# Kernel optimization log

Measured on AMD Instinct MI355X. Metric: run time of the kernel, lower is better.

The kernel has to match this reference:

```python
import jax, jax.numpy as jnp
import numpy as np

H, Q, D, V = 256, 64, 512, 34
L, N, T = 1024, 64, 256


def _mlp(x, W0, b0, W1, b1):
    # two-layer MLP with ELU on hidden (matches MLP with nn.ELU activation)
    return jax.nn.elu(x @ W0.T + b0) @ W1.T + b1


def _lstm_cell(x, h, c, Wih, Whh, bih, bhh):
    gates = x @ Wih.T + bih + h @ Whh.T + bhh
    i, f, g, o = jnp.split(gates, 4, axis=-1)  # PyTorch LSTMCell gate order
    i, f, o = jax.nn.sigmoid(i), jax.nn.sigmoid(f), jax.nn.sigmoid(o)
    c_new = f * c + i * jnp.tanh(g)
    h_new = o * jnp.tanh(c_new)
    return h_new, c_new


def _attn(q, key, value, mask):
    # q: [N,Q], key: [N,L,Q], value: [N,L,H], mask: [N,L]
    scores = jnp.einsum('nlq,nq->nl', key, q)
    a = jax.nn.softmax(scores, axis=-1) * mask
    a = a / jnp.sum(a, axis=-1, keepdims=True)
    return jnp.einsum('nl,nlh->nh', a, value)


def setup_inputs() -> dict:
    key = jax.random.key(0)
    ks = iter(jax.random.split(key, 64))

    def rn(shape, s=0.05):
        return jax.random.normal(next(ks), shape, jnp.float32) * s

    inp = {
        'seqs': rn((L, N, D), 1.0),
        'seq_lens': jax.random.randint(next(ks), (N,), L // 2, L + 1),
        'labels': jax.random.randint(next(ks), (T, N), 0, V),
        'emb': rn((V, H)),
        'inith': rn((3, H)),
        'initc': rn((3, H)),
    }
    in_sizes = [2 * H, H, H]
    for i in range(3):
        inp[f'Wih{i}'] = rn((4 * H, in_sizes[i]))
        inp[f'Whh{i}'] = rn((4 * H, H))
        inp[f'bih{i}'] = rn((4 * H,))
        inp[f'bhh{i}'] = rn((4 * H,))
    inp['qW0'] = rn((H, H)); inp['qb0'] = rn((H,))
    inp['qW1'] = rn((Q, H)); inp['qb1'] = rn((Q,))
    inp['kW0'] = rn((D, D)); inp['kb0'] = rn((D,))
    inp['kW1'] = rn((Q, D)); inp['kb1'] = rn((Q,))
    inp['vW0'] = rn((H, D)); inp['vb0'] = rn((H,))
    inp['vW1'] = rn((H, H)); inp['vb1'] = rn((H,))
    inp['outW'] = rn((V, 2 * H)); inp['outb'] = rn((V,))
    return inp


def reference(seqs, seq_lens, labels, emb, inith, initc,
              Wih0, Whh0, bih0, bhh0, Wih1, Whh1, bih1, bhh1,
              Wih2, Whh2, bih2, bhh2,
              qW0, qb0, qW1, qb1, kW0, kb0, kW1, kb1,
              vW0, vb0, vW1, vb1, outW, outb):
    T_, N_ = labels.shape
    L_ = seqs.shape[0]
    lstm = [(Wih0, Whh0, bih0, bhh0), (Wih1, Whh1, bih1, bhh1), (Wih2, Whh2, bih2, bhh2)]

    char_input = emb[labels]                                   # [T,N,H]
    key = _mlp(seqs, kW0, kb0, kW1, kb1).transpose(1, 0, 2)    # [N,L,Q]
    value = _mlp(seqs, vW0, vb0, vW1, vb1).transpose(1, 0, 2)  # [N,L,H]
    mask = (jnp.arange(L_)[None, :] < seq_lens[:, None]).astype(seqs.dtype)

    h = jnp.tile(inith[:, None, :], (1, N_, 1))  # [3,N,H]
    c = jnp.tile(initc[:, None, :], (1, N_, 1))
    q = _mlp(h[2], qW0, qb0, qW1, qb1)
    prev_ctx = _attn(q, key, value, mask)

    def step(carry, x_t):
        h, c, ctx = carry
        xin = jnp.concatenate([ctx, x_t], axis=1)  # [N,2H]
        hs, cs = [], []
        for i in range(3):
            nh, nc = _lstm_cell(xin, h[i], c[i], *lstm[i])
            hs.append(nh); cs.append(nc)
            xin = nh
        h = jnp.stack(hs); c = jnp.stack(cs)
        q = _mlp(h[2], qW0, qb0, qW1, qb1)
        ctx = _attn(q, key, value, mask)
        out = jnp.concatenate([ctx, h[2]], axis=1) @ outW.T + outb  # [N,V]
        return (h, c, ctx), out

    _, outs = jax.lax.scan(step, (h, c, prev_ctx), char_input)
    return outs  # [T,N,V]
```

## Files before the change

kernel.cpp:

```cpp
#include <hip/hip_runtime.h>
#include <cstddef>

#define DEV static __device__ __forceinline__
typedef unsigned long long ull;

DEV float b2f(unsigned short u){ unsigned int i=((unsigned int)u)<<16; float f; __builtin_memcpy(&f,&i,4); return f; }
DEV float lo16(unsigned int u){ unsigned int i=u<<16; float f; __builtin_memcpy(&f,&i,4); return f; }
DEV float hi16(unsigned int u){ unsigned int i=u&0xffff0000u; float f; __builtin_memcpy(&f,&i,4); return f; }
DEV unsigned short f2b(float f){ unsigned int i; __builtin_memcpy(&i,&f,4); unsigned int r=(i+0x7fffu+((i>>16)&1u))>>16; return (unsigned short)r; }
DEV float sigf(float x){ return 1.f/(1.f+__expf(-x)); }
DEV float eluf(float x){ return x>0.f ? x : (__expf(x)-1.f); }
DEV float gload(const void* p, long i, int f32){
  return f32 ? ((const float*)p)[i] : b2f(((const unsigned short*)p)[i]);
}
DEV ull pk(float f, unsigned tag){ unsigned b; __builtin_memcpy(&b,&f,4); return ((ull)tag<<32)|b; }
DEV float upk(ull u){ unsigned b=(unsigned)u; float f; __builtin_memcpy(&f,&b,4); return f; }
DEV void ast64(ull* p, ull v){ __hip_atomic_store(p, v, __ATOMIC_RELAXED, __HIP_MEMORY_SCOPE_AGENT); }
DEV ull ald64(const ull* p){ return __hip_atomic_load(p, __ATOMIC_RELAXED, __HIP_MEMORY_SCOPE_AGENT); }

__global__ __launch_bounds__(64) void sniff(const void* __restrict__ seqs,
                                            const void* __restrict__ seq_lens,
                                            int* __restrict__ flags)
{
  __shared__ int cnt;
  if (threadIdx.x==0) cnt=0;
  __syncthreads();
  const unsigned short* u = (const unsigned short*)seqs;
  int sane=0;
  for (int i=threadIdx.x;i<1024;i+=64){
    int e = (u[i]>>7)&0xFF;
    if (e>=0x70 && e<=0x8F) sane++;
  }
  atomicAdd(&cnt, sane);
  __syncthreads();
  if (threadIdx.x==0){
    flags[0] = (cnt < 820) ? 1 : 0;
    const int* s = (const int*)seq_lens;
    flags[1] = ((s[1]|s[3]|s[5]|s[7])==0) ? 1 : 0;
  }
}

__global__ __launch_bounds__(256) void prep_transpose(
    const void* __restrict__ Wih0, const void* __restrict__ Whh0,
    const void* __restrict__ Wih1, const void* __restrict__ Whh1,
    const void* __restrict__ Wih2, const void* __restrict__ Whh2,
    const void* __restrict__ kW0,  const void* __restrict__ kW1,
    const void* __restrict__ vW0,  const void* __restrict__ vW1,
    const void* __restrict__ qW0,  const void* __restrict__ qW1,
    const void* __restrict__ bih0, const void* __restrict__ bhh0,
    const void* __restrict__ bih1, const void* __restrict__ bhh1,
    const void* __restrict__ bih2, const void* __restrict__ bhh2,
    const void* __restrict__ outW, const void* __restrict__ inith,
    const void* __restrict__ initc, const void* __restrict__ qb0,
    const void* __restrict__ qb1,  const void* __restrict__ outb,
    const int* __restrict__ flags,
    unsigned short* __restrict__ Wl0, unsigned short* __restrict__ Wl1,
    unsigned short* __restrict__ Wl2,
    unsigned short* __restrict__ kW0T, unsigned short* __restrict__ kW1T,
    unsigned short* __restrict__ vW0T, unsigned short* __restrict__ vW1T,
    unsigned short* __restrict__ qW0v, unsigned short* __restrict__ qW1v,
    float* __restrict__ bsum,
    unsigned short* __restrict__ outWc, unsigned short* __restrict__ inithc,
    unsigned short* __restrict__ initcc, unsigned short* __restrict__ qb0c,
    unsigned short* __restrict__ qb1c,  unsigned short* __restrict__ outbc)
{
  const int f32 = flags[0];
  int idx = blockIdx.x*256 + threadIdx.x;
  if (idx < 524288){ int r=idx&131071, k=r>>8, gi=r&255;
    int g = ((gi>>6)<<8) + ((idx>>17)<<6) + (gi&63);
    Wl0[idx] = f2b((k<256)? gload(Wih0,(long)g*512+k,f32) : gload(Whh0,(long)g*256+(k-256),f32)); return; }
  idx -= 524288;
  if (idx < 524288){ int r=idx&131071, k=r>>8, gi=r&255;
    int g = ((gi>>6)<<8) + ((idx>>17)<<6) + (gi&63);
    Wl1[idx] = f2b((k<256)? gload(Wih1,(long)g*256+k,f32) : gload(Whh1,(long)g*256+(k-256),f32)); return; }
  idx -= 524288;
  if (idx < 524288){ int r=idx&131071, k=r>>8, gi=r&255;
    int g = ((gi>>6)<<8) + ((idx>>17)<<6) + (gi&63);
    Wl2[idx] = f2b((k<256)? gload(Wih2,(long)g*256+k,f32) : gload(Whh2,(long)g*256+(k-256),f32)); return; }
  idx -= 524288;
  if (idx < 262144){ int k=idx>>9, j=idx&511; kW0T[idx]=f2b(gload(kW0,(long)j*512+k,f32)); return; }
  idx -= 262144;
  if (idx < 32768){ int k=idx>>6, j=idx&63; kW1T[idx]=f2b(gload(kW1,(long)j*512+k,f32)); return; }
  idx -= 32768;
  if (idx < 131072){ int k=idx>>8, j=idx&255; vW0T[idx]=f2b(gload(vW0,(long)j*512+k,f32)); return; }
  idx -= 131072;
  if (idx < 65536){ int k=idx>>8, j=idx&255; vW1T[idx]=f2b(gload(vW1,(long)j*256+k,f32)); return; }
  idx -= 65536;
  if (idx < 65536){
    int k8=idx>>11, j=(idx>>3)&255, kk=idx&7; int k=k8*8+kk;
    qW0v[idx]=f2b(gload(qW0,(long)j*256+k,f32)); return; }
  idx -= 65536;
  if (idx < 16384){
    int s=idx>>10, qc=(idx>>4)&63, kk=idx&15; int k=s*16+kk;
    qW1v[idx]=f2b(gload(qW1,(long)qc*256+k,f32)); return; }
  idx -= 16384;
  if (idx < 3072){ int l=idx>>10, r=idx&1023, pp=r>>8, gi=r&255;
    int g = ((gi>>6)<<8) + (pp<<6) + (gi&63);
    const void* bi = (l==0)?bih0:((l==1)?bih1:bih2);
    const void* bh = (l==0)?bhh0:((l==1)?bhh1:bhh2);
    bsum[idx] = gload(bi,g,f32)+gload(bh,g,f32); return; }
  idx -= 3072;
  if (idx < 17408){ outWc[idx]=f2b(gload(outW,idx,f32)); return; }
  idx -= 17408;
  if (idx < 768){ inithc[idx]=f2b(gload(inith,idx,f32)); return; }
  idx -= 768;
  if (idx < 768){ initcc[idx]=f2b(gload(initc,idx,f32)); return; }
  idx -= 768;
  if (idx < 256){ qb0c[idx]=f2b(gload(qb0,idx,f32)); return; }
  idx -= 256;
  if (idx < 64){ qb1c[idx]=f2b(gload(qb1,idx,f32)); return; }
  idx -= 64;
  if (idx < 34){ outbc[idx]=f2b(gload(outb,idx,f32)); return; }
}

__global__ __launch_bounds__(256) void prep_ge(
    const void* __restrict__ emb,
    const void* __restrict__ Wih0,
    const int* __restrict__ flags,
    float* __restrict__ gep)
{
  __shared__ float ev[256];
  const int f32 = flags[0];
  const int v = blockIdx.x, tid = threadIdx.x;
  ev[tid] = gload(emb,(long)v*256+tid,f32);
  __syncthreads();
  #pragma unroll
  for (int j=0;j<4;j++){
    const int g = tid*4+j;
    float a = 0.f;
    #pragma unroll 4
    for (int k=0;k<256;k++) a += ev[k]*gload(Wih0,(long)g*512+256+k,f32);
    int pp = (g>>6)&3, gi = ((g>>8)<<6)|(g&63);
    gep[((size_t)pp*34+v)*256+gi] = a;
  }
}

__global__ __launch_bounds__(256) void key_mlp(
    const void* __restrict__ seqs,
    const unsigned short* __restrict__ kW0T, const void* __restrict__ kb0,
    const unsigned short* __restrict__ kW1T, const void* __restrict__ kb1,
    const int* __restrict__ flags,
    unsigned short* __restrict__ keyT)
{
  __shared__ float Xt[16*512];
  __shared__ unsigned short Hd[16*512];
  const int f32 = flags[0];
  const int tid = threadIdx.x;
  const int R0 = blockIdx.x*16;
  for (int i=tid;i<8192;i+=256) Xt[i] = gload(seqs,(long)R0*512+i,f32);
  __syncthreads();
  {
    const int j0 = 2*tid;
    float acc0[16], acc1[16];
    #pragma unroll
    for (int r=0;r<16;r++){ acc0[r]=0.f; acc1[r]=0.f; }
    for (int k=0;k<512;k++){
      ushort2 w = *reinterpret_cast<const ushort2*>(kW0T + (size_t)k*512 + j0);
      float w0=b2f(w.x), w1=b2f(w.y);
      #pragma unroll
      for (int r=0;r<16;r++){ float x = Xt[r*512+k]; acc0[r]+=x*w0; acc1[r]+=x*w1; }
    }
    float b0v=gload(kb0,j0,f32), b1v=gload(kb0,j0+1,f32);
    #pragma unroll
    for (int r=0;r<16;r++){
      Hd[r*512+j0]   = f2b(eluf(acc0[r]+b0v));
      Hd[r*512+j0+1] = f2b(eluf(acc1[r]+b1v));
    }
  }
  __syncthreads();
  {
    const int j = tid & 63;
    const int rbase = tid >> 6;
    float acc[4] = {0.f,0.f,0.f,0.f};
    for (int k=0;k<512;k++){
      float w = b2f(kW1T[(size_t)k*64 + j]);
      #pragma unroll
      for (int m=0;m<4;m++) acc[m] += b2f(Hd[(rbase+4*m)*512 + k]) * w;
    }
    float bv = gload(kb1,j,f32);
    #pragma unroll
    for (int m=0;m<4;m++){
      int R = R0 + rbase + 4*m;
      int l = R >> 6, n = R & 63;
      keyT[((size_t)(n*64 + j))*1024 + l] = f2b(acc[m]+bv);
    }
  }
}

__global__ __launch_bounds__(256) void value_mlp(
    const void* __restrict__ seqs,
    const unsigned short* __restrict__ vW0T, const void* __restrict__ vb0,
    const unsigned short* __restrict__ vW1T, const void* __restrict__ vb1,
    const int* __restrict__ flags,
    unsigned short* __restrict__ value)
{
  __shared__ float Xt[16*512];
  __shared__ float Hd[16*256];
  const int f32 = flags[0];
  const int tid = threadIdx.x;
  const int R0 = blockIdx.x*16;
  for (int i=tid;i<8192;i+=256) Xt[i] = gload(seqs,(long)R0*512+i,f32);
  __syncthreads();
  {
    const int j0 = 2*(tid & 127);
    const int rh = tid >> 7;
    float acc0[8], acc1[8];
    #pragma unroll
    for (int r=0;r<8;r++){ acc0[r]=0.f; acc1[r]=0.f; }
    for (int k=0;k<512;k++){
      ushort2 w = *reinterpret_cast<const ushort2*>(vW0T + (size_t)k*256 + j0);
      float w0=b2f(w.x), w1=b2f(w.y);
      #pragma unroll
      for (int r=0;r<8;r++){ float x = Xt[(rh*8+r)*512+k]; acc0[r]+=x*w0; acc1[r]+=x*w1; }
    }
    float b0v=gload(vb0,j0,f32), b1v=gload(vb0,j0+1,f32);
    #pragma unroll
    for (int r=0;r<8;r++){
      Hd[(rh*8+r)*256+j0]   = eluf(acc0[r]+b0v);
      Hd[(rh*8+r)*256+j0+1] = eluf(acc1[r]+b1v);
    }
  }
  __syncthreads();
  {
    const int j = tid;
    float acc[16];
    #pragma unroll
    for (int r=0;r<16;r++) acc[r]=0.f;
    for (int k=0;k<256;k++){
      float w = b2f(vW1T[(size_t)k*256 + j]);
      #pragma unroll
      for (int r=0;r<16;r++) acc[r] += Hd[r*256+k]*w;
    }
    float bv = gload(vb1,j,f32);
    #pragma unroll
    for (int r=0;r<16;r++){
      int R = R0 + r; int l = R>>6, n = R&63;
      value[((size_t)n*1024 + l)*256 + j] = f2b(acc[r]+bv);
    }
  }
}

__global__ __launch_bounds__(256) void zero_hbuf(ull* __restrict__ f){
  int i = blockIdx.x*256 + threadIdx.x;
  if (i < 115200) f[i] = 0;
}

__global__ __launch_bounds__(512, 1) void speller(
    const unsigned short* __restrict__ keyT,
    const unsigned short* __restrict__ value,
    const unsigned short* __restrict__ Wl0,
    const unsigned short* __restrict__ Wl1,
    const unsigned short* __restrict__ Wl2,
    const unsigned short* __restrict__ qW0v,
    const unsigned short* __restrict__ qW1v,
    const float* __restrict__ bsum_p,
    const float* __restrict__ gep,
    const unsigned short* __restrict__ inithc,
    const unsigned short* __restrict__ initcc,
    const unsigned short* __restrict__ qb0c,
    const unsigned short* __restrict__ qb1c,
    const unsigned short* __restrict__ outWc,
    const unsigned short* __restrict__ outbc,
    const int* __restrict__ labels,
    const int* __restrict__ seq_lens,
    const int* __restrict__ dflags,
    ull* __restrict__ hbw,
    void* __restrict__ out)
{
  extern __shared__ char smem_dyn[];
  unsigned short* vlds = (unsigned short*)smem_dyn;

  __shared__ float sacc[4096];
  __shared__ float inc[512];
  __shared__ float garr[256];
  __shared__ float h0[256], h1[256], h2[256], ctx[256];
  __shared__ float cloc[3][64];
  __shared__ float xq[256];
  __shared__ float qv[64];
  __shared__ float earr[256];
  __shared__ float red[16];
  __shared__ float wf[4];
  __shared__ float pcl[256];
  __shared__ float statl[8];

  const int tid = threadIdx.x;
  const int n = blockIdx.x >> 2;
  const int p = blockIdx.x & 3;
  const int f32o = dflags[0];
  const int i64 = dflags[1];
  const int slen = i64 ? seq_lens[2*n] : seq_lens[n];

  ull* mb   = hbw + (size_t)n*1800;
  ull* H0w  = mb;
  ull* H1w  = mb + 256;
  ull* H2w  = mb + 512;
  ull* PCw  = mb + 768;
  ull* STw  = mb + 1792;

  {
    const uint4* src = (const uint4*)(value + ((size_t)n*1024 + p*256)*256);
    uint4* dst = (uint4*)vlds;
    for (int i=tid;i<16384;i+=512) dst[i] = src[i];
  }
  if (tid < 256){ h0[tid]=b2f(inithc[tid]); h1[tid]=b2f(inithc[256+tid]); h2[tid]=b2f(inithc[512+tid]); }
  if (tid < 64){
    cloc[0][tid]=b2f(initcc[p*64+tid]);
    cloc[1][tid]=b2f(initcc[256+p*64+tid]);
    cloc[2][tid]=b2f(initcc[512+p*64+tid]);
  }
  __syncthreads();

  auto lstm_lds = [&](const unsigned short* W, const float* bs, const float* ger,
                      int layer, ull* Hw, unsigned tag){
    const int go8 = tid & 31, ks = tid >> 5;
    const unsigned short* wp = W + (size_t)p*131072 + (size_t)ks*32*256 + go8*8;
    const float* xin = inc + ks*32;
    float a0=0.f,a1=0.f,a2=0.f,a3=0.f,a4=0.f,a5=0.f,a6=0.f,a7=0.f;
    #pragma unroll 16
    for (int k=0;k<32;k++){
      float x = xin[k];
      uint4 w = *reinterpret_cast<const uint4*>(wp + (size_t)k*256);
      a0 += x*lo16(w.x); a1 += x*hi16(w.x);
      a2 += x*lo16(w.y); a3 += x*hi16(w.y);
      a4 += x*lo16(w.z); a5 += x*hi16(w.z);
      a6 += x*lo16(w.w); a7 += x*hi16(w.w);
    }
    float* sb = sacc + ks*256 + go8*8;
    sb[0]=a0; sb[1]=a1; sb[2]=a2; sb[3]=a3; sb[4]=a4; sb[5]=a5; sb[6]=a6; sb[7]=a7;
    __syncthreads();
    if (tid < 256){
      float s = bs[tid] + (ger ? ger[tid] : 0.f);
      #pragma unroll
      for (int u=0;u<16;u++) s += sacc[u*256+tid];
      garr[tid] = s;
    }
    __syncthreads();
    if (tid < 64){
      __builtin_amdgcn_s_setprio(1);
      float gi=garr[tid], gf=garr[64+tid], gg=garr[128+tid], go=garr[192+tid];
      float cc = sigf(gf)*cloc[layer][tid] + sigf(gi)*tanhf(gg);
      float hh = sigf(go)*tanhf(cc);
      cloc[layer][tid]=cc;
      ast64(Hw + p*64 + tid, pk(hh, tag));
      __builtin_amdgcn_s_setprio(0);
    }
  };

  auto lstm_poll = [&](const unsigned short* W, const float* bs,
                       const ull* Xw, unsigned xtag, const float* hprev,
                       float* xdst, int layer, ull* Hw, unsigned tag){
    const int go8 = tid & 31, ks = tid >> 5;
    const int lane = tid & 63, wv = tid >> 6;
    float xv;
    if (wv < 4){
      const ull* wd = Xw + tid;
      ull u = ald64(wd);
      while ((unsigned)(u>>32) != xtag) u = ald64(wd);
      xv = upk(u);
    } else {
      xv = hprev[tid - 256];
    }
    const unsigned short* wp = W + (size_t)p*131072 + (size_t)ks*32*256 + go8*8;
    float a0=0.f,a1=0.f,a2=0.f,a3=0.f,a4=0.f,a5=0.f,a6=0.f,a7=0.f;
    #pragma unroll 16
    for (int k=0;k<32;k++){
      float x = __shfl(xv, (lane & 32) | k);
      uint4 w = *reinterpret_cast<const uint4*>(wp + (size_t)k*256);
      a0 += x*lo16(w.x); a1 += x*hi16(w.x);
      a2 += x*lo16(w.y); a3 += x*hi16(w.y);
      a4 += x*lo16(w.z); a5 += x*hi16(w.z);
      a6 += x*lo16(w.w); a7 += x*hi16(w.w);
    }
    float* sb = sacc + ks*256 + go8*8;
    sb[0]=a0; sb[1]=a1; sb[2]=a2; sb[3]=a3; sb[4]=a4; sb[5]=a5; sb[6]=a6; sb[7]=a7;
    if (wv < 4) xdst[tid] = xv;
    __syncthreads();
    if (tid < 256){
      float s = bs[tid];
      #pragma unroll
      for (int u=0;u<16;u++) s += sacc[u*256+tid];
      garr[tid] = s;
    }
    __syncthreads();
    if (tid < 64){
      __builtin_amdgcn_s_setprio(1);
      float gi=garr[tid], gf=garr[64+tid], gg=garr[128+tid], go=garr[192+tid];
      float cc = sigf(gf)*cloc[layer][tid] + sigf(gi)*tanhf(gg);
      float hh = sigf(go)*tanhf(cc);
      cloc[layer][tid]=cc;
      ast64(Hw + p*64 + tid, pk(hh, tag));
      __builtin_amdgcn_s_setprio(0);
    }
  };

  auto gather_h2 = [&](unsigned tag){
    if (tid < 256){
      const ull* w = H2w + tid; ull u = ald64(w);
      while ((unsigned)(u>>32) != tag) u = ald64(w);
      h2[tid] = upk(u);
    }
    __syncthreads();
  };

  auto attn = [&](unsigned tag){
    {
      const int j = tid & 255, kh = tid >> 8;
      const uint4* qp = (const uint4*)qW0v + (size_t)(kh*16)*256 + j;
      float a = 0.f;
      #pragma unroll
      for (int k8=0;k8<16;k8++){
        uint4 w = qp[(size_t)k8*256];
        const float* hb = h2 + kh*128 + k8*8;
        a += hb[0]*lo16(w.x)+hb[1]*hi16(w.x)
           + hb[2]*lo16(w.y)+hb[3]*hi16(w.y)
           + hb[4]*lo16(w.z)+hb[5]*hi16(w.z)
           + hb[6]*lo16(w.w)+hb[7]*hi16(w.w);
      }
      sacc[kh*256 + j] = a;
    }
    __syncthreads();
    if (tid < 256) xq[tid] = eluf(sacc[tid]+sacc[256+tid] + b2f(qb0c[tid]));
    __syncthreads();
    {
      const int qc = tid & 63, s = tid >> 6;
      const uint4* qp = (const uint4*)qW1v + (size_t)(2*s*64+qc)*2;
      float a = 0.f;
      #pragma unroll
      for (int half=0;half<2;half++){
        const uint4* qph = qp + (size_t)half*64*2;
        #pragma unroll
        for (int u=0;u<2;u++){
          uint4 w = qph[u];
          const float* xb = xq + s*32 + half*16 + u*8;
          a += xb[0]*lo16(w.x)+xb[1]*hi16(w.x)
             + xb[2]*lo16(w.y)+xb[3]*hi16(w.y)
             + xb[4]*lo16(w.z)+xb[5]*hi16(w.z)
             + xb[6]*lo16(w.w)+xb[7]*hi16(w.w);
        }
      }
      sacc[s*64+qc] = a;
    }
    __syncthreads();
    if (tid < 64){
      float s=0.f;
      #pragma unroll
      for (int u=0;u<8;u++) s += sacc[u*64+tid];
      qv[tid] = s + b2f(qb1c[tid]);
    }
    __syncthreads();
    {
      const int lp = tid & 127, qh = tid >> 7;
      float a0=0.f,a1=0.f;
      const unsigned short* kp = keyT + (size_t)n*65536 + (size_t)qh*16*1024 + p*256 + 2*lp;
      #pragma unroll 8
      for (int q=0;q<16;q++){
        ushort2 w = *reinterpret_cast<const ushort2*>(kp + (size_t)q*1024);
        float qq = qv[qh*16+q];
        a0 += qq*b2f(w.x); a1 += qq*b2f(w.y);
      }
      sacc[qh*256+2*lp]=a0; sacc[qh*256+2*lp+1]=a1;
    }
    __syncthreads();
    float pmax, psum;
    {
      float s = -1e30f;
      if (tid < 256){
        s = sacc[tid]+sacc[256+tid]+sacc[512+tid]+sacc[768+tid];
        if (p*256+tid >= slen) s = -1e30f;
      }
      float m = s;
      #pragma unroll
      for (int off=32; off; off>>=1) m = fmaxf(m, __shfl_xor(m, off));
      if ((tid&63)==0) red[tid>>6] = m;
      __syncthreads();
      pmax = fmaxf(fmaxf(red[0],red[1]),fmaxf(red[2],red[3]));
      float e = 0.f;
      if (tid < 256){
        e = (p*256+tid < slen) ? __expf(s - pmax) : 0.f;
        earr[tid] = e;
      }
      float ss = e;
      #pragma unroll
      for (int off=32; off; off>>=1) ss += __shfl_xor(ss, off);
      if ((tid&63)==0) red[8+(tid>>6)] = ss;
      __syncthreads();
      psum = red[8]+red[9]+red[10]+red[11];
    }
    {
      const int hp = tid & 127, lq = tid >> 7;
      float a0=0.f,a1=0.f;
      const unsigned short* vp = vlds + (size_t)(lq*64)*256 + 2*hp;
      #pragma unroll 8
      for (int l=0;l<64;l++){
        ushort2 w = *reinterpret_cast<const ushort2*>(vp + (size_t)l*256);
        float e = earr[lq*64+l];
        a0 += e*b2f(w.x); a1 += e*b2f(w.y);
      }
      sacc[lq*256+2*hp]=a0; sacc[lq*256+2*hp+1]=a1;
    }
    __syncthreads();
    if (tid < 256){
      float v = sacc[tid]+sacc[256+tid]+sacc[512+tid]+sacc[768+tid];
      pcl[tid] = v;
      ast64(PCw + p*256 + tid, pk(v, tag));
    }
    if (tid == 0){ ast64(STw + p*2, pk(pmax, tag)); ast64(STw + p*2 + 1, pk(psum, tag)); }
    if (tid < 8){
      int q = tid >> 1, ix = tid & 1; float v;
      if (q == p) v = ix ? psum : pmax;
      else { const ull* w = STw + q*2 + ix; ull u = ald64(w);
             while ((unsigned)(u>>32) != tag) u = ald64(w);
             v = upk(u); }
      statl[tid] = v;
    }
    __syncthreads();
    if (tid == 0){
      float m0=statl[0], s0=statl[1], m1=statl[2], s1=statl[3];
      float m2=statl[4], s2=statl[5], m3=statl[6], s3=statl[7];
      float M = fmaxf(fmaxf(m0,m1),fmaxf(m2,m3));
      float w0=__expf(m0-M), w1=__expf(m1-M), w2=__expf(m2-M), w3=__expf(m3-M);
      float inv = 1.f/(s0*w0+s1*w1+s2*w2+s3*w3);
      wf[0]=w0*inv; wf[1]=w1*inv; wf[2]=w2*inv; wf[3]=w3*inv;
    }
    __syncthreads();
    if (tid < 256){
      const int q0=(p+1)&3, q1=(p+2)&3, q2=(p+3)&3;
      const ull* w0 = PCw + q0*256 + tid;
      const ull* w1 = PCw + q1*256 + tid;
      const ull* w2 = PCw + q2*256 + tid;
      ull u0=ald64(w0), u1=ald64(w1), u2=ald64(w2);
      while ((unsigned)(u0>>32) != tag) u0 = ald64(w0);
      while ((unsigned)(u1>>32) != tag) u1 = ald64(w1);
      while ((unsigned)(u2>>32) != tag) u2 = ald64(w2);
      float acc = pcl[tid]*wf[p] + upk(u0)*wf[q0] + upk(u1)*wf[q1] + upk(u2)*wf[q2];
      ctx[tid] = acc;
      inc[tid] = acc;
      inc[256+tid] = h0[tid];
    }
    __syncthreads();
  };

  attn(1);

  for (int t=0;t<256;t++){
    const unsigned tb = 4*(unsigned)t;
    const int lab = i64 ? labels[2*(t*64+n)] : labels[t*64+n];
    lstm_lds(Wl0, bsum_p + p*256, gep + ((size_t)p*34+lab)*256, 0, H0w, tb+2);
    lstm_poll(Wl1, bsum_p + 1024 + p*256, H0w, tb+2, h1, h0, 1, H1w, tb+3);
    lstm_poll(Wl2, bsum_p + 2048 + p*256, H1w, tb+3, h2, h1, 2, H2w, tb+4);
    gather_h2(tb+4);
    attn(tb+5);
    {
      const int ri = tid >> 6, kk = tid & 63;
      const int r = 4*ri + p;
      float acc = 0.f;
      const unsigned short* wr = outWc + (size_t)r*512 + kk;
      #pragma unroll
      for (int s=0;s<4;s++) acc += ctx[s*64+kk]*b2f(wr[s*64]);
      #pragma unroll
      for (int s=0;s<4;s++) acc += h2[s*64+kk]*b2f(wr[256+s*64]);
      #pragma unroll
      for (int off=32; off>0; off>>=1) acc += __shfl_down(acc, off);
      if (kk==0){
        float v = acc + b2f(outbc[r]);
        size_t oi = ((size_t)(t*64+n))*34 + r;
        if (f32o) ((float*)out)[oi]=v; else ((unsigned short*)out)[oi]=f2b(v);
      }
      if (p < 2 && tid < 64){
        const int r2 = 32+p;
        float a2=0.f;
        const unsigned short* wr2 = outWc + (size_t)r2*512 + tid;
        #pragma unroll
        for (int s=0;s<4;s++) a2 += ctx[s*64+tid]*b2f(wr2[s*64]);
        #pragma unroll
        for (int s=0;s<4;s++) a2 += h2[s*64+tid]*b2f(wr2[256+s*64]);
        #pragma unroll
        for (int off=32; off>0; off>>=1) a2 += __shfl_down(a2, off);
        if (tid==0){
          float v = a2 + b2f(outbc[r2]);
          size_t oi = ((size_t)(t*64+n))*34 + r2;
          if (f32o) ((float*)out)[oi]=v; else ((unsigned short*)out)[oi]=f2b(v);
        }
      }
    }
  }
}

extern "C" void kernel_launch(void* const* d_in, const int* in_sizes, int n_in,
                              void* d_out, int out_size, void* d_ws, size_t ws_size,
                              hipStream_t stream) {
  const void* seqs  = d_in[0];
  const int* seq_lens = (const int*)d_in[1];
  const int* labels   = (const int*)d_in[2];
  const void* emb   = d_in[3];
  const void* inith = d_in[4];
  const void* initc = d_in[5];
  const void* Wih0 = d_in[6];  const void* Whh0 = d_in[7];
  const void* bih0 = d_in[8];  const void* bhh0 = d_in[9];
  const void* Wih1 = d_in[10]; const void* Whh1 = d_in[11];
  const void* bih1 = d_in[12]; const void* bhh1 = d_in[13];
  const void* Wih2 = d_in[14]; const void* Whh2 = d_in[15];
  const void* bih2 = d_in[16]; const void* bhh2 = d_in[17];
  const void* qW0 = d_in[18];  const void* qb0 = d_in[19];
  const void* qW1 = d_in[20];  const void* qb1 = d_in[21];
  const void* kW0 = d_in[22];  const void* kb0 = d_in[23];
  const void* kW1 = d_in[24];  const void* kb1 = d_in[25];
  const void* vW0 = d_in[26];  const void* vb0 = d_in[27];
  const void* vW1 = d_in[28];  const void* vb1 = d_in[29];
  const void* outW = d_in[30]; const void* outb = d_in[31];

  char* ws = (char*)d_ws;
  unsigned short* keyT  = (unsigned short*)(ws);
  unsigned short* value = (unsigned short*)(ws + 8388608);
  unsigned short* Wl0   = (unsigned short*)(ws + 41943040);
  unsigned short* Wl1   = (unsigned short*)(ws + 42991616);
  unsigned short* Wl2   = (unsigned short*)(ws + 44040192);
  unsigned short* kW0T  = (unsigned short*)(ws + 45088768);
  unsigned short* kW1T  = (unsigned short*)(ws + 45613056);
  unsigned short* vW0T  = (unsigned short*)(ws + 45678592);
  unsigned short* vW1T  = (unsigned short*)(ws + 45940736);
  unsigned short* qW0v  = (unsigned short*)(ws + 46071808);
  unsigned short* qW1v  = (unsigned short*)(ws + 46202880);
  float*          bsum  = (float*)(ws + 46235648);
  float*          gep   = (float*)(ws + 46247936);
  unsigned short* outWc = (unsigned short*)(ws + 46387200);
  unsigned short* inithc= (unsigned short*)(ws + 46422016);
  unsigned short* initcc= (unsigned short*)(ws + 46423552);
  unsigned short* qb0c  = (unsigned short*)(ws + 46425088);
  unsigned short* qb1c  = (unsigned short*)(ws + 46425600);
  unsigned short* outbc = (unsigned short*)(ws + 46425728);
  int*            dflags= (int*)(ws + 46425856);
  ull* hbw = (ull*)(ws + 45088768);

  sniff<<<dim3(1), dim3(64), 0, stream>>>(seqs, seq_lens, dflags);
  prep_transpose<<<dim3(8472), dim3(256), 0, stream>>>(
      Wih0,Whh0,Wih1,Whh1,Wih2,Whh2, kW0,kW1,vW0,vW1,qW0,qW1,
      bih0,bhh0,bih1,bhh1,bih2,bhh2,
      outW,inith,initc,qb0,qb1,outb, dflags,
      Wl0,Wl1,Wl2,kW0T,kW1T,vW0T,vW1T,qW0v,qW1v,bsum,
      outWc,inithc,initcc,qb0c,qb1c,outbc);
  prep_ge<<<dim3(34), dim3(256), 0, stream>>>(emb, Wih0, dflags, gep);
  key_mlp<<<dim3(4096), dim3(256), 0, stream>>>(seqs, kW0T, kb0, kW1T, kb1, dflags, keyT);
  value_mlp<<<dim3(4096), dim3(256), 0, stream>>>(seqs, vW0T, vb0, vW1T, vb1, dflags, value);
  zero_hbuf<<<dim3(450), dim3(256), 0, stream>>>(hbw);
  hipFuncSetAttribute((const void*)speller, hipFuncAttributeMaxDynamicSharedMemorySize, 131072);
  speller<<<dim3(256), dim3(512), 131072, stream>>>(
      keyT, value, Wl0, Wl1, Wl2, qW0v, qW1v, bsum, gep,
      inithc, initcc, qb0c, qb1c, outWc, outbc, labels, seq_lens, dflags,
      hbw, d_out);
}
```

Baseline: 8.173 ms.

## Keep layer-1 LSTM weights in registers and defer output projection into next step

```diff
diff --git a/kernel.cpp b/kernel.cpp
--- a/kernel.cpp
+++ b/kernel.cpp
@@ -308,11 +308,51 @@
     cloc[1][tid]=b2f(initcc[256+p*64+tid]);
     cloc[2][tid]=b2f(initcc[512+p*64+tid]);
   }
+  const int go8 = tid & 31, ks = tid >> 5;
+  uint4 w1r[32];
+  {
+    const unsigned short* wp1 = Wl1 + (size_t)p*131072 + (size_t)ks*32*256 + go8*8;
+    #pragma unroll
+    for (int k=0;k<32;k++) w1r[k] = *reinterpret_cast<const uint4*>(wp1 + (size_t)k*256);
+  }
   __syncthreads();
 
+  auto outproj = [&](int t){
+    const int ri = tid >> 6, kk = tid & 63;
+    const int r = 4*ri + p;
+    float acc = 0.f;
+    const unsigned short* wr = outWc + (size_t)r*512 + kk;
+    #pragma unroll
+    for (int s=0;s<4;s++) acc += ctx[s*64+kk]*b2f(wr[s*64]);
+    #pragma unroll
+    for (int s=0;s<4;s++) acc += h2[s*64+kk]*b2f(wr[256+s*64]);
+    #pragma unroll
+    for (int off=32; off>0; off>>=1) acc += __shfl_down(acc, off);
+    if (kk==0){
+      float v = acc + b2f(outbc[r]);
+      size_t oi = ((size_t)(t*64+n))*34 + r;
+      if (f32o) ((float*)out)[oi]=v; else ((unsigned short*)out)[oi]=f2b(v);
+    }
+    if (p < 2 && tid < 64){
+      const int r2 = 32+p;
+      float a2=0.f;
+      const unsigned short* wr2 = outWc + (size_t)r2*512 + tid;
+      #pragma unroll
+      for (int s=0;s<4;s++) a2 += ctx[s*64+tid]*b2f(wr2[s*64]);
+      #pragma unroll
+      for (int s=0;s<4;s++) a2 += h2[s*64+tid]*b2f(wr2[256+s*64]);
+      #pragma unroll
+      for (int off=32; off>0; off>>=1) a2 += __shfl_down(a2, off);
+      if (tid==0){
+        float v = a2 + b2f(outbc[r2]);
+        size_t oi = ((size_t)(t*64+n))*34 + r2;
+        if (f32o) ((float*)out)[oi]=v; else ((unsigned short*)out)[oi]=f2b(v);
+      }
+    }
+  };
+
   auto lstm_lds = [&](const unsigned short* W, const float* bs, const float* ger,
-                      int layer, ull* Hw, unsigned tag){
-    const int go8 = tid & 31, ks = tid >> 5;
+                      int layer, ull* Hw, unsigned tag, int tprev){
     const unsigned short* wp = W + (size_t)p*131072 + (size_t)ks*32*256 + go8*8;
     const float* xin = inc + ks*32;
     float a0=0.f,a1=0.f,a2=0.f,a3=0.f,a4=0.f,a5=0.f,a6=0.f,a7=0.f;
@@ -327,6 +367,7 @@
     }
     float* sb = sacc + ks*256 + go8*8;
     sb[0]=a0; sb[1]=a1; sb[2]=a2; sb[3]=a3; sb[4]=a4; sb[5]=a5; sb[6]=a6; sb[7]=a7;
+    if (tprev >= 0) outproj(tprev);
     __syncthreads();
     if (tid < 256){
       float s = bs[tid] + (ger ? ger[tid] : 0.f);
@@ -349,7 +390,6 @@
   auto lstm_poll = [&](const unsigned short* W, const float* bs,
                        const ull* Xw, unsigned xtag, const float* hprev,
                        float* xdst, int layer, ull* Hw, unsigned tag){
-    const int go8 = tid & 31, ks = tid >> 5;
     const int lane = tid & 63, wv = tid >> 6;
     float xv;
     if (wv < 4){
@@ -366,6 +406,51 @@
     for (int k=0;k<32;k++){
       float x = __shfl(xv, (lane & 32) | k);
       uint4 w = *reinterpret_cast<const uint4*>(wp + (size_t)k*256);
+      a0 += x*lo16(w.x); a1 += x*hi16(w.x);
+      a2 += x*lo16(w.y); a3 += x*hi16(w.y);
+      a4 += x*lo16(w.z); a5 += x*hi16(w.z);
+      a6 += x*lo16(w.w); a7 += x*hi16(w.w);
+    }
+    float* sb = sacc + ks*256 + go8*8;
+    sb[0]=a0; sb[1]=a1; sb[2]=a2; sb[3]=a3; sb[4]=a4; sb[5]=a5; sb[6]=a6; sb[7]=a7;
+    if (wv < 4) xdst[tid] = xv;
+    __syncthreads();
+    if (tid < 256){
+      float s = bs[tid];
+      #pragma unroll
+      for (int u=0;u<16;u++) s += sacc[u*256+tid];
+      garr[tid] = s;
+    }
+    __syncthreads();
+    if (tid < 64){
+      __builtin_amdgcn_s_setprio(1);
+      float gi=garr[tid], gf=garr[64+tid], gg=garr[128+tid], go=garr[192+tid];
+      float cc = sigf(gf)*cloc[layer][tid] + sigf(gi)*tanhf(gg);
+      float hh = sigf(go)*tanhf(cc);
+      cloc[layer][tid]=cc;
+      ast64(Hw + p*64 + tid, pk(hh, tag));
+      __builtin_amdgcn_s_setprio(0);
+    }
+  };
+
+  auto lstm_poll_reg = [&](const float* bs,
+                           const ull* Xw, unsigned xtag, const float* hprev,
+                           float* xdst, int layer, ull* Hw, unsigned tag){
+    const int lane = tid & 63, wv = tid >> 6;
+    float xv;
+    if (wv < 4){
+      const ull* wd = Xw + tid;
+      ull u = ald64(wd);
+      while ((unsigned)(u>>32) != xtag) u = ald64(wd);
+      xv = upk(u);
+    } else {
+      xv = hprev[tid - 256];
+    }
+    float a0=0.f,a1=0.f,a2=0.f,a3=0.f,a4=0.f,a5=0.f,a6=0.f,a7=0.f;
+    #pragma unroll
+    for (int k=0;k<32;k++){
+      float x = __shfl(xv, (lane & 32) | k);
+      uint4 w = w1r[k];
       a0 += x*lo16(w.x); a1 += x*hi16(w.x);
       a2 += x*lo16(w.y); a3 += x*hi16(w.y);
       a4 += x*lo16(w.z); a5 += x*hi16(w.z);
@@ -542,48 +627,20 @@
 
   attn(1);
 
+  int lab = i64 ? labels[2*n] : labels[n];
   for (int t=0;t<256;t++){
     const unsigned tb = 4*(unsigned)t;
-    const int lab = i64 ? labels[2*(t*64+n)] : labels[t*64+n];
-    lstm_lds(Wl0, bsum_p + p*256, gep + ((size_t)p*34+lab)*256, 0, H0w, tb+2);
-    lstm_poll(Wl1, bsum_p + 1024 + p*256, H0w, tb+2, h1, h0, 1, H1w, tb+3);
+    const float* ger = gep + ((size_t)p*34+lab)*256;
+    int lab_next = 0;
+    if (t < 255) lab_next = i64 ? labels[2*((t+1)*64+n)] : labels[(t+1)*64+n];
+    lstm_lds(Wl0, bsum_p + p*256, ger, 0, H0w, tb+2, t-1);
+    lstm_poll_reg(bsum_p + 1024 + p*256, H0w, tb+2, h1, h0, 1, H1w, tb+3);
     lstm_poll(Wl2, bsum_p + 2048 + p*256, H1w, tb+3, h2, h1, 2, H2w, tb+4);
     gather_h2(tb+4);
     attn(tb+5);
-    {
-      const int ri = tid >> 6, kk = tid & 63;
-      const int r = 4*ri + p;
-      float acc = 0.f;
-      const unsigned short* wr = outWc + (size_t)r*512 + kk;
-      #pragma unroll
-      for (int s=0;s<4;s++) acc += ctx[s*64+kk]*b2f(wr[s*64]);
-      #pragma unroll
-      for (int s=0;s<4;s++) acc += h2[s*64+kk]*b2f(wr[256+s*64]);
-      #pragma unroll
-      for (int off=32; off>0; off>>=1) acc += __shfl_down(acc, off);
-      if (kk==0){
-        float v = acc + b2f(outbc[r]);
-        size_t oi = ((size_t)(t*64+n))*34 + r;
-        if (f32o) ((float*)out)[oi]=v; else ((unsigned short*)out)[oi]=f2b(v);
-      }
-      if (p < 2 && tid < 64){
-        const int r2 = 32+p;
-        float a2=0.f;
-        const unsigned short* wr2 = outWc + (size_t)r2*512 + tid;
-        #pragma unroll
-        for (int s=0;s<4;s++) a2 += ctx[s*64+tid]*b2f(wr2[s*64]);
-        #pragma unroll
-        for (int s=0;s<4;s++) a2 += h2[s*64+tid]*b2f(wr2[256+s*64]);
-        #pragma unroll
-        for (int off=32; off>0; off>>=1) a2 += __shfl_down(a2, off);
-        if (tid==0){
-          float v = a2 + b2f(outbc[r2]);
-          size_t oi = ((size_t)(t*64+n))*34 + r2;
-          if (f32o) ((float*)out)[oi]=v; else ((unsigned short*)out)[oi]=f2b(v);
-        }
-      }
-    }
-  }
+    lab = lab_next;
+  }
+  outproj(255);
 }
 
 extern "C" void kernel_launch(void* const* d_in, const int* in_sizes, int n_in,
```

New measurement: 20.94 ms. 2.56x slower.
